# Kernel optimization log

Measured on AMD Instinct MI355X. Metric: run time of the kernel, lower is better.

## Reference

```python
import jax, jax.numpy as jnp
import numpy as np

B, D_IN, D_OUT, E = 8192, 1024, 1024, 16


def setup_inputs() -> dict:
    key = jax.random.key(0)
    k1, k2, k3 = jax.random.split(key, 3)
    x = jax.random.normal(k1, (B, D_IN), dtype=jnp.float32)
    Wg = jax.random.normal(k2, (D_IN, E), dtype=jnp.float32) * (1.0 / np.sqrt(D_IN))
    bg = jnp.zeros((E,), dtype=jnp.float32)
    We = jax.random.normal(k3, (E, D_IN, D_OUT), dtype=jnp.float32) * (1.0 / np.sqrt(D_IN))
    be = jnp.zeros((E, D_OUT), dtype=jnp.float32)
    return {"x": x, "Wg": Wg, "bg": bg, "We": We, "be": be}


def reference(x, Wg, bg, We, be):
    # Gate: [B, E]
    gate_out = x @ Wg + bg
    top1 = jnp.argmax(gate_out, axis=1)  # [B]
    # All-expert dense compute (faithful to the naive HardMoE): [B, E, D_OUT]
    expert_outs = jnp.einsum('bd,edh->beh', x, We) + be[None, :, :]
    # Gather each row's argmax expert output: [B, D_OUT]
    out = jnp.take_along_axis(expert_outs, top1[:, None, None], axis=1)[:, 0, :]
    return out
```

## Files before the change

### kernel.cpp

```cpp
#include <hip/hip_runtime.h>

typedef unsigned short u16;
typedef __attribute__((ext_vector_type(4))) unsigned short u16x4;
typedef __attribute__((ext_vector_type(8))) short short8;
typedef __attribute__((ext_vector_type(4))) float floatx4;

#define NB 8192
#define DK 1024
#define DN 1024
#define NE 16
#define TM 128
#define TN 128
#define BK 128
#define MAX_TILES 80
#define GTHR 4e-3f

#define GATE_BLOCKS 512
#define WET_BLOCKS  4096

__device__ __forceinline__ u16 f2bf(float f) {
    union { float f; unsigned int u; } v; v.f = f;
    unsigned int u = v.u;
    return (u16)((u + 0x7fffu + ((u >> 16) & 1u)) >> 16);
}

__device__ __forceinline__ float bf2f(u16 h) {
    union { unsigned int u; float f; } v; v.u = ((unsigned int)h) << 16;
    return v.f;
}

__device__ __forceinline__ void gld16(const void* g, void* l) {
    __builtin_amdgcn_global_load_lds(
        (const __attribute__((address_space(1))) unsigned int*)g,
        (__attribute__((address_space(3))) unsigned int*)l, 16, 0, 0);
}

__global__ __launch_bounds__(256) void k_prep(const float* __restrict__ x,
                                              const float* __restrict__ Wg,
                                              const float* __restrict__ bg,
                                              const float* __restrict__ We,
                                              u16* __restrict__ xb,
                                              u16* __restrict__ WeT,
                                              int* __restrict__ cnt,
                                              int* __restrict__ bucket,
                                              int* __restrict__ fixcnt,
                                              int* __restrict__ fixlist) {
    __shared__ union {
        struct {
            u16 xsh[4][16 * 64];
            u16 xsl[4][16 * 64];
            u16 wgh[4][16 * 64];
            u16 wgl[4][16 * 64];
            float gred[4][16 * 17];
        } g;
        float t[64 * 65];
    } sh;

    const int tid = threadIdx.x;

    if (blockIdx.x < GATE_BLOCKS) {
        const int lane = tid & 63;
        const int w = tid >> 6;
        const int lr = lane & 15, q = lane >> 4;
        const int R0 = blockIdx.x * 16;
        const int kw = w * 256;

        floatx4 acc = (floatx4)0.0f;

        for (int cc = 0; cc < 4; ++cc) {
            const int kc = kw + cc * 64;
            #pragma unroll
            for (int i = 0; i < 2; ++i) {
                int c = i * 64 + lane;
                int r = c >> 3, s8 = c & 7;
                const float* gp = &x[(size_t)(R0 + r) * DK + kc + s8 * 8];
                float4 v0 = *(const float4*)gp;
                float4 v1 = *(const float4*)(gp + 4);
                float vv[8] = { v0.x, v0.y, v0.z, v0.w, v1.x, v1.y, v1.z, v1.w };
                u16 hi[8], lo[8];
                #pragma unroll
                for (int j = 0; j < 8; ++j) {
                    hi[j] = f2bf(vv[j]);
                    lo[j] = f2bf(vv[j] - bf2f(hi[j]));
                }
                int a = r * 64 + ((s8 ^ (r & 7)) * 8);
                *(short8*)&sh.g.xsh[w][a] = *(const short8*)hi;
                *(short8*)&sh.g.xsl[w][a] = *(const short8*)lo;
                *(short8*)&xb[(size_t)(R0 + r) * DK + kc + s8 * 8] = *(const short8*)hi;
            }
            #pragma unroll
            for (int i = 0; i < 4; ++i) {
                int f = i * 64 + lane;
                int k = f >> 2;
                int e4 = (f & 3) * 4;
                float4 v = *(const float4*)&Wg[(size_t)(kc + k) * NE + e4];
                int s = k >> 3, j = k & 7;
                float vv[4] = { v.x, v.y, v.z, v.w };
                #pragma unroll
                for (int t2 = 0; t2 < 4; ++t2) {
                    int er = e4 + t2;
                    u16 hi = f2bf(vv[t2]);
                    u16 lo = f2bf(vv[t2] - bf2f(hi));
                    int a = er * 64 + ((s ^ (er & 7)) * 8 + j);
                    sh.g.wgh[w][a] = hi;
                    sh.g.wgl[w][a] = lo;
                }
            }
            __syncthreads();
            #pragma unroll
            for (int kwin = 0; kwin < 2; ++kwin) {
                int sg = kwin * 4 + q;
                int ab = lr * 64 + ((sg ^ (lr & 7)) * 8);
                short8 bh = *(const short8*)&sh.g.wgh[w][ab];
                short8 bl = *(const short8*)&sh.g.wgl[w][ab];
                short8 ah = *(const short8*)&sh.g.xsh[w][ab];
                short8 al = *(const short8*)&sh.g.xsl[w][ab];
                acc = __builtin_amdgcn_mfma_f32_16x16x32_bf16(ah, bh, acc, 0, 0, 0);
                acc = __builtin_amdgcn_mfma_f32_16x16x32_bf16(ah, bl, acc, 0, 0, 0);
                acc = __builtin_amdgcn_mfma_f32_16x16x32_bf16(al, bh, acc, 0, 0, 0);
            }
            __syncthreads();
        }

        #pragma unroll
        for (int rr = 0; rr < 4; ++rr)
            sh.g.gred[w][(q * 4 + rr) * 17 + lr] = acc[rr];
        __syncthreads();

        if (tid < 16) {
            int row = R0 + tid;
            float g[16];
            #pragma unroll
            for (int e = 0; e < 16; ++e)
                g[e] = sh.g.gred[0][tid * 17 + e] + sh.g.gred[1][tid * 17 + e]
                     + sh.g.gred[2][tid * 17 + e] + sh.g.gred[3][tid * 17 + e] + bg[e];
            float best = g[0], second = -1e30f; int bi = 0;
            #pragma unroll
            for (int e = 1; e < 16; ++e) {
                if (g[e] > best) { second = best; best = g[e]; bi = e; }
                else if (g[e] > second) second = g[e];
            }
            if (best - second >= GTHR) {
                int pos = atomicAdd(&cnt[bi], 1);
                bucket[bi * NB + pos] = row;
            } else {
                int f = atomicAdd(fixcnt, 1);
                fixlist[f] = row;
            }
        }
    } else {
        const int bw = blockIdx.x - GATE_BLOCKS;
        const int e  = bw >> 8;
        const int n0 = ((bw >> 4) & 15) * 64;
        const int k0 = (bw & 15) * 64;
        const float* src = We + (size_t)e * DK * DN;
        float* t = sh.t;

        const int n4 = (tid & 15) * 4;
        const int kl = tid >> 4;
        #pragma unroll
        for (int r = 0; r < 4; ++r) {
            int k = r * 16 + kl;
            float4 v = *(const float4*)&src[(size_t)(k0 + k) * DN + n0 + n4];
            t[k * 65 + n4 + 0] = v.x;
            t[k * 65 + n4 + 1] = v.y;
            t[k * 65 + n4 + 2] = v.z;
            t[k * 65 + n4 + 3] = v.w;
        }
        __syncthreads();
        u16* dst = WeT + (size_t)e * DN * DK;
        #pragma unroll
        for (int r = 0; r < 2; ++r) {
            int idx = r * 256 + tid;
            int nl = idx >> 3;
            int k8 = idx & 7;
            u16 pk[8];
            #pragma unroll
            for (int i = 0; i < 8; ++i)
                pk[i] = f2bf(t[(k8 * 8 + i) * 65 + nl]);
            *(short8*)&dst[(size_t)(n0 + nl) * DK + k0 + k8 * 8] = *(const short8*)pk;
        }
    }
}

__global__ __launch_bounds__(256) void k_fix(const float* __restrict__ x,
                                             const float* __restrict__ Wg,
                                             const float* __restrict__ bg,
                                             const int* __restrict__ fixcnt,
                                             const int* __restrict__ fixlist,
                                             int* __restrict__ cnt,
                                             int* __restrict__ bucket) {
    __shared__ double lred[4][16];
    const int tid = threadIdx.x;
    const int lane = tid & 63;
    const int w = tid >> 6;
    const int n = *fixcnt;
    for (int it = blockIdx.x; it < n; it += 256) {
        const int row = fixlist[it];
        float4 xv = *(const float4*)&x[(size_t)row * DK + tid * 4];
        const float* xf = (const float*)&xv;
        double acc[16];
        #pragma unroll
        for (int e = 0; e < 16; ++e) acc[e] = 0.0;
        #pragma unroll
        for (int j = 0; j < 4; ++j) {
            int k = tid * 4 + j;
            double xd = (double)xf[j];
            const float4* wr = (const float4*)&Wg[(size_t)k * NE];
            float4 w0 = wr[0], w1 = wr[1], w2 = wr[2], w3 = wr[3];
            acc[0]  += xd * (double)w0.x;  acc[1]  += xd * (double)w0.y;
            acc[2]  += xd * (double)w0.z;  acc[3]  += xd * (double)w0.w;
            acc[4]  += xd * (double)w1.x;  acc[5]  += xd * (double)w1.y;
            acc[6]  += xd * (double)w1.z;  acc[7]  += xd * (double)w1.w;
            acc[8]  += xd * (double)w2.x;  acc[9]  += xd * (double)w2.y;
            acc[10] += xd * (double)w2.z;  acc[11] += xd * (double)w2.w;
            acc[12] += xd * (double)w3.x;  acc[13] += xd * (double)w3.y;
            acc[14] += xd * (double)w3.z;  acc[15] += xd * (double)w3.w;
        }
        #pragma unroll
        for (int e = 0; e < 16; ++e) {
            double v = acc[e];
            #pragma unroll
            for (int off = 1; off < 64; off <<= 1)
                v += __shfl_xor(v, off);
            acc[e] = v;
        }
        if (lane == 0) {
            #pragma unroll
            for (int e = 0; e < 16; ++e) lred[w][e] = acc[e];
        }
        __syncthreads();
        if (tid == 0) {
            double best = -1e300; int bi = 0;
            #pragma unroll
            for (int e = 0; e < 16; ++e) {
                double g = lred[0][e] + lred[1][e] + lred[2][e] + lred[3][e]
                         + (double)bg[e];
                if (g > best) { best = g; bi = e; }
            }
            int pos = atomicAdd(&cnt[bi], 1);
            bucket[bi * NB + pos] = row;
        }
        __syncthreads();
    }
}

__global__ __launch_bounds__(256) void k_moe(const u16* __restrict__ xb,
                                             const u16* __restrict__ WeT,
                                             const float* __restrict__ be,
                                             const int* __restrict__ bucket,
                                             const int* __restrict__ cnt,
                                             float* __restrict__ out) {
    const int slot = blockIdx.x >> 3;
    const int nt = blockIdx.x & 7;

    int e = -1, mt = 0, cntE = 0, acc_t = 0;
    #pragma unroll
    for (int ee = 0; ee < NE; ++ee) {
        int ce = cnt[ee];
        int nte = (ce + TM - 1) / TM;
        if (e < 0 && slot < acc_t + nte) { e = ee; mt = slot - acc_t; cntE = ce; }
        acc_t += nte;
    }
    if (e < 0) return;

    const int m0 = mt * TM;
    const int n0 = nt * TN;

    __shared__ u16 aLds[TM * BK];
    __shared__ u16 bLds[TN * BK];

    const int tid = threadIdx.x;
    const int lane = tid & 63;
    const int w = tid >> 6;
    const int wr = w >> 1, wc = w & 1;
    const int lr = lane & 15, q = lane >> 4;

    long aoff[8]; long boff[8]; int ldsb[8];
    #pragma unroll
    for (int r = 0; r < 8; ++r) {
        int c = r * 256 + tid;
        int row = c >> 4;
        int k16 = (c & 15) ^ (row & 15);
        int m_idx = m0 + row; if (m_idx >= cntE) m_idx = cntE - 1;
        long rid = bucket[e * NB + m_idx];
        aoff[r] = rid * DK + k16 * 8;
        boff[r] = (long)e * DN * DK + (long)(n0 + row) * DK + k16 * 8;
        ldsb[r] = (r * 256 + (tid & ~63)) * 8;
    }

    floatx4 acc[4][4];
    #pragma unroll
    for (int mi = 0; mi < 4; ++mi)
        #pragma unroll
        for (int ni = 0; ni < 4; ++ni)
            acc[mi][ni] = (floatx4)0.0f;

    for (int kk = 0; kk < DK; kk += BK) {
        #pragma unroll
        for (int r = 0; r < 8; ++r)
            gld16(xb + aoff[r] + kk, &aLds[ldsb[r]]);
        #pragma unroll
        for (int r = 0; r < 8; ++r)
            gld16(WeT + boff[r] + kk, &bLds[ldsb[r]]);
        __syncthreads();
        #pragma unroll
        for (int ks = 0; ks < 4; ++ks) {
            const int kt = ks * 4 + q;
            short8 af[4], bfr[4];
            #pragma unroll
            for (int mi = 0; mi < 4; ++mi) {
                int row = wr * 64 + mi * 16 + lr;
                af[mi] = *(const short8*)&aLds[row * BK + ((kt ^ (row & 15)) * 8)];
                int nrow = wc * 64 + mi * 16 + lr;
                bfr[mi] = *(const short8*)&bLds[nrow * BK + ((kt ^ (nrow & 15)) * 8)];
            }
            #pragma unroll
            for (int mi = 0; mi < 4; ++mi)
                #pragma unroll
                for (int ni = 0; ni < 4; ++ni)
                    acc[mi][ni] = __builtin_amdgcn_mfma_f32_16x16x32_bf16(
                        af[mi], bfr[ni], acc[mi][ni], 0, 0, 0);
        }
        __syncthreads();
    }

    float bias[4];
    #pragma unroll
    for (int ni = 0; ni < 4; ++ni)
        bias[ni] = be[e * DN + n0 + wc * 64 + ni * 16 + lr];

    #pragma unroll
    for (int mi = 0; mi < 4; ++mi) {
        #pragma unroll
        for (int rr = 0; rr < 4; ++rr) {
            int row_l = wr * 64 + mi * 16 + q * 4 + rr;
            int m_idx = m0 + row_l;
            if (m_idx < cntE) {
                long rid = bucket[e * NB + m_idx];
                float* orow = out + rid * DN + n0 + wc * 64 + lr;
                #pragma unroll
                for (int ni = 0; ni < 4; ++ni)
                    orow[ni * 16] = acc[mi][ni][rr] + bias[ni];
            }
        }
    }
}

extern "C" void kernel_launch(void* const* d_in, const int* in_sizes, int n_in,
                              void* d_out, int out_size, void* d_ws, size_t ws_size,
                              hipStream_t stream) {
    const float* x  = (const float*)d_in[0];
    const float* Wg = (const float*)d_in[1];
    const float* bg = (const float*)d_in[2];
    const float* We = (const float*)d_in[3];
    const float* be = (const float*)d_in[4];
    float* out = (float*)d_out;

    int* cnt     = (int*)d_ws;
    int* fixcnt  = cnt + 16;
    int* fixlist = cnt + 32;
    int* bucket  = cnt + 8448;
    u16* xb  = (u16*)((char*)d_ws + (1u << 20));
    u16* wet = (u16*)((char*)d_ws + (18u << 20));

    hipMemsetAsync(cnt, 0, 20 * sizeof(int), stream);
    k_prep<<<GATE_BLOCKS + WET_BLOCKS, 256, 0, stream>>>(x, Wg, bg, We, xb, wet,
                                                         cnt, bucket, fixcnt, fixlist);
    k_fix<<<256, 256, 0, stream>>>(x, Wg, bg, fixcnt, fixlist, cnt, bucket);
    k_moe<<<MAX_TILES * 8, 256, 0, stream>>>(xb, wet, be, bucket, cnt, out);
}
```

Measured before the change: 216.8 us.

## Drop LDS staging in prep kernel and halve GEMM K-tile to 64

```diff
diff --git a/kernel.cpp b/kernel.cpp
--- a/kernel.cpp
+++ b/kernel.cpp
@@ -1,7 +1,6 @@
 #include <hip/hip_runtime.h>
 
 typedef unsigned short u16;
-typedef __attribute__((ext_vector_type(4))) unsigned short u16x4;
 typedef __attribute__((ext_vector_type(8))) short short8;
 typedef __attribute__((ext_vector_type(4))) float floatx4;
 
@@ -11,7 +10,7 @@
 #define NE 16
 #define TM 128
 #define TN 128
-#define BK 128
+#define BK 64
 #define MAX_TILES 80
 #define GTHR 4e-3f
 
@@ -35,26 +34,17 @@
         (__attribute__((address_space(3))) unsigned int*)l, 16, 0, 0);
 }
 
-__global__ __launch_bounds__(256) void k_prep(const float* __restrict__ x,
-                                              const float* __restrict__ Wg,
-                                              const float* __restrict__ bg,
-                                              const float* __restrict__ We,
-                                              u16* __restrict__ xb,
-                                              u16* __restrict__ WeT,
-                                              int* __restrict__ cnt,
-                                              int* __restrict__ bucket,
-                                              int* __restrict__ fixcnt,
-                                              int* __restrict__ fixlist) {
-    __shared__ union {
-        struct {
-            u16 xsh[4][16 * 64];
-            u16 xsl[4][16 * 64];
-            u16 wgh[4][16 * 64];
-            u16 wgl[4][16 * 64];
-            float gred[4][16 * 17];
-        } g;
-        float t[64 * 65];
-    } sh;
+__global__ __launch_bounds__(256, 4) void k_prep(const float* __restrict__ x,
+                                                 const float* __restrict__ Wg,
+                                                 const float* __restrict__ bg,
+                                                 const float* __restrict__ We,
+                                                 u16* __restrict__ xb,
+                                                 u16* __restrict__ WeT,
+                                                 int* __restrict__ cnt,
+                                                 int* __restrict__ bucket,
+                                                 int* __restrict__ fixcnt,
+                                                 int* __restrict__ fixlist) {
+    __shared__ float gred[4][16 * 17];
 
     const int tid = threadIdx.x;
 
@@ -63,68 +53,49 @@
         const int w = tid >> 6;
         const int lr = lane & 15, q = lane >> 4;
         const int R0 = blockIdx.x * 16;
-        const int kw = w * 256;
+        const size_t xrow = (size_t)(R0 + lr) * DK;
 
         floatx4 acc = (floatx4)0.0f;
 
         for (int cc = 0; cc < 4; ++cc) {
-            const int kc = kw + cc * 64;
-            #pragma unroll
-            for (int i = 0; i < 2; ++i) {
-                int c = i * 64 + lane;
-                int r = c >> 3, s8 = c & 7;
-                const float* gp = &x[(size_t)(R0 + r) * DK + kc + s8 * 8];
+            const int kc = w * 256 + cc * 64;
+            #pragma unroll
+            for (int kwin = 0; kwin < 2; ++kwin) {
+                const int kb = kc + kwin * 32 + q * 8;
+                const float* gp = &x[xrow + kb];
                 float4 v0 = *(const float4*)gp;
                 float4 v1 = *(const float4*)(gp + 4);
-                float vv[8] = { v0.x, v0.y, v0.z, v0.w, v1.x, v1.y, v1.z, v1.w };
-                u16 hi[8], lo[8];
+                float av[8] = { v0.x, v0.y, v0.z, v0.w, v1.x, v1.y, v1.z, v1.w };
+                u16 ah[8], al[8];
                 #pragma unroll
                 for (int j = 0; j < 8; ++j) {
-                    hi[j] = f2bf(vv[j]);
-                    lo[j] = f2bf(vv[j] - bf2f(hi[j]));
+                    ah[j] = f2bf(av[j]);
+                    al[j] = f2bf(av[j] - bf2f(ah[j]));
                 }
-                int a = r * 64 + ((s8 ^ (r & 7)) * 8);
-                *(short8*)&sh.g.xsh[w][a] = *(const short8*)hi;
-                *(short8*)&sh.g.xsl[w][a] = *(const short8*)lo;
-                *(short8*)&xb[(size_t)(R0 + r) * DK + kc + s8 * 8] = *(const short8*)hi;
-            }
-            #pragma unroll
-            for (int i = 0; i < 4; ++i) {
-                int f = i * 64 + lane;
-                int k = f >> 2;
-                int e4 = (f & 3) * 4;
-                float4 v = *(const float4*)&Wg[(size_t)(kc + k) * NE + e4];
-                int s = k >> 3, j = k & 7;
-                float vv[4] = { v.x, v.y, v.z, v.w };
-                #pragma unroll
-                for (int t2 = 0; t2 < 4; ++t2) {
-                    int er = e4 + t2;
-                    u16 hi = f2bf(vv[t2]);
-                    u16 lo = f2bf(vv[t2] - bf2f(hi));
-                    int a = er * 64 + ((s ^ (er & 7)) * 8 + j);
-                    sh.g.wgh[w][a] = hi;
-                    sh.g.wgl[w][a] = lo;
+                *(short8*)&xb[xrow + kb] = *(const short8*)ah;
+                float wv[8];
+                #pragma unroll
+                for (int j = 0; j < 8; ++j)
+                    wv[j] = Wg[(size_t)(kb + j) * NE + lr];
+                u16 bh[8], bl[8];
+                #pragma unroll
+                for (int j = 0; j < 8; ++j) {
+                    bh[j] = f2bf(wv[j]);
+                    bl[j] = f2bf(wv[j] - bf2f(bh[j]));
                 }
-            }
-            __syncthreads();
-            #pragma unroll
-            for (int kwin = 0; kwin < 2; ++kwin) {
-                int sg = kwin * 4 + q;
-                int ab = lr * 64 + ((sg ^ (lr & 7)) * 8);
-                short8 bh = *(const short8*)&sh.g.wgh[w][ab];
-                short8 bl = *(const short8*)&sh.g.wgl[w][ab];
-                short8 ah = *(const short8*)&sh.g.xsh[w][ab];
-                short8 al = *(const short8*)&sh.g.xsl[w][ab];
-                acc = __builtin_amdgcn_mfma_f32_16x16x32_bf16(ah, bh, acc, 0, 0, 0);
-                acc = __builtin_amdgcn_mfma_f32_16x16x32_bf16(ah, bl, acc, 0, 0, 0);
-                acc = __builtin_amdgcn_mfma_f32_16x16x32_bf16(al, bh, acc, 0, 0, 0);
-            }
-            __syncthreads();
+                const short8 ahv = *(const short8*)ah;
+                const short8 alv = *(const short8*)al;
+                const short8 bhv = *(const short8*)bh;
+                const short8 blv = *(const short8*)bl;
+                acc = __builtin_amdgcn_mfma_f32_16x16x32_bf16(ahv, bhv, acc, 0, 0, 0);
+                acc = __builtin_amdgcn_mfma_f32_16x16x32_bf16(ahv, blv, acc, 0, 0, 0);
+                acc = __builtin_amdgcn_mfma_f32_16x16x32_bf16(alv, bhv, acc, 0, 0, 0);
+            }
         }
 
         #pragma unroll
         for (int rr = 0; rr < 4; ++rr)
-            sh.g.gred[w][(q * 4 + rr) * 17 + lr] = acc[rr];
+            gred[w][(q * 4 + rr) * 17 + lr] = acc[rr];
         __syncthreads();
 
         if (tid < 16) {
@@ -132,8 +103,8 @@
             float g[16];
             #pragma unroll
             for (int e = 0; e < 16; ++e)
-                g[e] = sh.g.gred[0][tid * 17 + e] + sh.g.gred[1][tid * 17 + e]
-                     + sh.g.gred[2][tid * 17 + e] + sh.g.gred[3][tid * 17 + e] + bg[e];
+                g[e] = gred[0][tid * 17 + e] + gred[1][tid * 17 + e]
+                     + gred[2][tid * 17 + e] + gred[3][tid * 17 + e] + bg[e];
             float best = g[0], second = -1e30f; int bi = 0;
             #pragma unroll
             for (int e = 1; e < 16; ++e) {
@@ -150,35 +121,21 @@
         }
     } else {
         const int bw = blockIdx.x - GATE_BLOCKS;
-        const int e  = bw >> 8;
-        const int n0 = ((bw >> 4) & 15) * 64;
-        const int k0 = (bw & 15) * 64;
-        const float* src = We + (size_t)e * DK * DN;
-        float* t = sh.t;
-
-        const int n4 = (tid & 15) * 4;
-        const int kl = tid >> 4;
-        #pragma unroll
-        for (int r = 0; r < 4; ++r) {
-            int k = r * 16 + kl;
-            float4 v = *(const float4*)&src[(size_t)(k0 + k) * DN + n0 + n4];
-            t[k * 65 + n4 + 0] = v.x;
-            t[k * 65 + n4 + 1] = v.y;
-            t[k * 65 + n4 + 2] = v.z;
-            t[k * 65 + n4 + 3] = v.w;
-        }
-        __syncthreads();
-        u16* dst = WeT + (size_t)e * DN * DK;
-        #pragma unroll
-        for (int r = 0; r < 2; ++r) {
-            int idx = r * 256 + tid;
-            int nl = idx >> 3;
-            int k8 = idx & 7;
+        const int w = tid >> 6;
+        const int lane = tid & 63;
+        #pragma unroll
+        for (int t = 0; t < 2; ++t) {
+            const int task = bw * 8 + w * 2 + t;
+            const int ngrp = task & 15;
+            const int kc   = (task >> 4) & 127;
+            const int e    = task >> 11;
+            const int n    = ngrp * 64 + lane;
+            const float* src = We + ((size_t)e * DK + (size_t)kc * 8) * DN + n;
             u16 pk[8];
             #pragma unroll
             for (int i = 0; i < 8; ++i)
-                pk[i] = f2bf(t[(k8 * 8 + i) * 65 + nl]);
-            *(short8*)&dst[(size_t)(n0 + nl) * DK + k0 + k8 * 8] = *(const short8*)pk;
+                pk[i] = f2bf(src[(size_t)i * DN]);
+            *(short8*)&WeT[((size_t)e * DN + n) * DK + kc * 8] = *(const short8*)pk;
         }
     }
 }
@@ -276,12 +233,12 @@
     const int wr = w >> 1, wc = w & 1;
     const int lr = lane & 15, q = lane >> 4;
 
-    long aoff[8]; long boff[8]; int ldsb[8];
-    #pragma unroll
-    for (int r = 0; r < 8; ++r) {
+    long aoff[4]; long boff[4]; int ldsb[4];
+    #pragma unroll
+    for (int r = 0; r < 4; ++r) {
         int c = r * 256 + tid;
-        int row = c >> 4;
-        int k16 = (c & 15) ^ (row & 15);
+        int row = c >> 3;
+        int k16 = (c & 7) ^ (row & 7);
         int m_idx = m0 + row; if (m_idx >= cntE) m_idx = cntE - 1;
         long rid = bucket[e * NB + m_idx];
         aoff[r] = rid * DK + k16 * 8;
@@ -298,22 +255,22 @@
 
     for (int kk = 0; kk < DK; kk += BK) {
         #pragma unroll
-        for (int r = 0; r < 8; ++r)
+        for (int r = 0; r < 4; ++r)
             gld16(xb + aoff[r] + kk, &aLds[ldsb[r]]);
         #pragma unroll
-        for (int r = 0; r < 8; ++r)
+        for (int r = 0; r < 4; ++r)
             gld16(WeT + boff[r] + kk, &bLds[ldsb[r]]);
         __syncthreads();
         #pragma unroll
-        for (int ks = 0; ks < 4; ++ks) {
-            const int kt = ks * 4 + q;
+        for (int kwin = 0; kwin < 2; ++kwin) {
+            const int sl = kwin * 4 + q;
             short8 af[4], bfr[4];
             #pragma unroll
             for (int mi = 0; mi < 4; ++mi) {
                 int row = wr * 64 + mi * 16 + lr;
-                af[mi] = *(const short8*)&aLds[row * BK + ((kt ^ (row & 15)) * 8)];
+                af[mi] = *(const short8*)&aLds[row * BK + ((sl ^ (row & 7)) * 8)];
                 int nrow = wc * 64 + mi * 16 + lr;
-                bfr[mi] = *(const short8*)&bLds[nrow * BK + ((kt ^ (nrow & 15)) * 8)];
+                bfr[mi] = *(const short8*)&bLds[nrow * BK + ((sl ^ (nrow & 7)) * 8)];
             }
             #pragma unroll
             for (int mi = 0; mi < 4; ++mi)
```

Result: slower. 230.6 us (+6.4%).
